# Optimization experiments

Hardware: AMD Instinct MI355X
Metric: run time of the kernel (lower is better)

## Reference

```python
import jax, jax.numpy as jnp
import numpy as np
import math

B, L, D, H = 2, 2048, 1024, 16
HD = D // H

def setup_inputs() -> dict:
    key = jax.random.key(0)
    ks = jax.random.split(key, 8)
    s = 1.0 / math.sqrt(D)
    # causal additive mask: 0 on/below diagonal, -inf above
    causal = jnp.where(jnp.tril(jnp.ones((L, L), dtype=bool)), 0.0, -jnp.inf)
    causal = causal[None, None].astype(jnp.float32)  # [1,1,L,L]
    return {
        "Q": jax.random.normal(ks[0], (B, L, D), jnp.float32),
        "K": jax.random.normal(ks[1], (B, L, D), jnp.float32),
        "V": jax.random.normal(ks[2], (B, L, D), jnp.float32),
        "attn_mask": causal,
        "padding_mask": jnp.zeros((B, L), dtype=bool),
        "wq": jax.random.normal(ks[3], (D, D), jnp.float32) * s,
        "wk": jax.random.normal(ks[4], (D, D), jnp.float32) * s,
        "wv": jax.random.normal(ks[5], (D, D), jnp.float32) * s,
        "wout": jax.random.normal(ks[6], (D, D), jnp.float32) * s,
    }

def reference(Q, K, V, attn_mask, padding_mask, wq, wk, wv, wout):
    b, l, _ = Q.shape
    # projections (torch Linear: x @ W.T); weights sampled as [out,in]-like square
    def proj(x, w):
        return (x @ w.T).reshape(b, l, H, HD).transpose(0, 2, 1, 3)  # [B,H,L,hd]
    q = proj(Q, wq)
    k = proj(K, wk)
    v = proj(V, wv)
    scores = jnp.einsum("bhqd,bhkd->bhqk", q, k) / math.sqrt(HD)
    scores = scores + attn_mask
    scores = jnp.where(padding_mask[:, None, None, :], -jnp.inf, scores)
    weights = jax.nn.softmax(scores, axis=-1)
    ctx = jnp.einsum("bhqk,bhkd->bhqd", weights, v)
    ctx = ctx.transpose(0, 2, 1, 3).reshape(b, l, D)
    return ctx @ wout.T
```

## Files before the change

kernel.cpp:

```cpp
#include <hip/hip_runtime.h>
#include <stdint.h>
#include <stddef.h>

typedef __bf16 bf16_t;
typedef bf16_t bf16x4 __attribute__((ext_vector_type(4)));
typedef bf16_t bf16x8 __attribute__((ext_vector_type(8)));
typedef float f32x4 __attribute__((ext_vector_type(4)));
typedef uint32_t u32x2 __attribute__((ext_vector_type(2)));
typedef uint32_t u32x4 __attribute__((ext_vector_type(4)));

#define MFMA_BF16(A_, B_, C_) __builtin_amdgcn_mfma_f32_16x16x32_bf16(A_, B_, C_, 0, 0, 0)

static constexpr int Lseq = 2048;
static constexpr int Dmod = 1024;
static constexpr int Hn   = 16;
static constexpr int HDim = 64;
static constexpr size_t M1 = 1u << 20;

__device__ __forceinline__ int swz(int row, int chunk) {
  return row * 64 + ((chunk ^ (row & 7)) << 3);
}

__device__ __forceinline__ void async_ld16(const bf16_t* g, bf16_t* l) {
  __builtin_amdgcn_global_load_lds(
      (const __attribute__((address_space(1))) void*)g,
      (__attribute__((address_space(3))) void*)l, 16, 0, 0);
}

__device__ __forceinline__ bf16x8 xpose(uint32_t a0, uint32_t a1,
                                        uint32_t b0, uint32_t b1,
                                        int s0, int s1, bool lo) {
  uint32_t ua0 = (uint32_t)__shfl((int)a0, s0, 64);
  uint32_t ub0 = (uint32_t)__shfl((int)b0, s0, 64);
  uint32_t ua1 = (uint32_t)__shfl((int)a1, s0, 64);
  uint32_t ub1 = (uint32_t)__shfl((int)b1, s0, 64);
  uint32_t va0 = (uint32_t)__shfl((int)a0, s1, 64);
  uint32_t vb0 = (uint32_t)__shfl((int)b0, s1, 64);
  uint32_t va1 = (uint32_t)__shfl((int)a1, s1, 64);
  uint32_t vb1 = (uint32_t)__shfl((int)b1, s1, 64);
  u32x4 t;
  t[0] = lo ? ua0 : ub0;
  t[1] = lo ? ua1 : ub1;
  t[2] = lo ? va0 : vb0;
  t[3] = lo ? va1 : vb1;
  return __builtin_bit_cast(bf16x8, t);
}

__device__ __forceinline__ u32x2 pack4(float e0, float e1, float e2, float e3) {
  bf16x4 p;
  p[0] = (bf16_t)e0; p[1] = (bf16_t)e1; p[2] = (bf16_t)e2; p[3] = (bf16_t)e3;
  return __builtin_bit_cast(u32x2, p);
}

__global__ __launch_bounds__(256) void cvt_kernel(
    const float* __restrict__ Q, const float* __restrict__ K,
    const float* __restrict__ V, const float* __restrict__ wq,
    const float* __restrict__ wk, const float* __restrict__ wv,
    const float* __restrict__ wout, bf16_t* __restrict__ wsb)
{
  const int s = blockIdx.z;
  const float* __restrict__ src;
  if      (s < 4)   src = Q    + (size_t)s * M1;
  else if (s < 8)   src = K    + (size_t)(s - 4) * M1;
  else if (s < 12)  src = V    + (size_t)(s - 8) * M1;
  else if (s == 12) src = wq;
  else if (s == 13) src = wk;
  else if (s == 14) src = wv;
  else              src = wout;
  bf16_t* __restrict__ dst = wsb + (size_t)s * M1;
  const float scale = (s == 12) ? 0.18033688f : 1.0f;

  const int idx = blockIdx.x * 256 + threadIdx.x;
  float4 a = ((const float4*)src)[idx * 2];
  float4 b = ((const float4*)src)[idx * 2 + 1];
  bf16x8 o;
  o[0] = (bf16_t)(a.x * scale); o[1] = (bf16_t)(a.y * scale);
  o[2] = (bf16_t)(a.z * scale); o[3] = (bf16_t)(a.w * scale);
  o[4] = (bf16_t)(b.x * scale); o[5] = (bf16_t)(b.y * scale);
  o[6] = (bf16_t)(b.z * scale); o[7] = (bf16_t)(b.w * scale);
  ((bf16x8*)dst)[idx] = o;
}

__global__ __launch_bounds__(256) void proj_kernel(
    const bf16_t* __restrict__ Qbf, const bf16_t* __restrict__ Kbf,
    const bf16_t* __restrict__ Vbf, const bf16_t* __restrict__ wqb,
    const bf16_t* __restrict__ wkb, const bf16_t* __restrict__ wvb,
    bf16_t* __restrict__ qo, bf16_t* __restrict__ ko, bf16_t* __restrict__ vo)
{
  const int z = blockIdx.z;
  const bf16_t* __restrict__ A  = (z == 0) ? Qbf : (z == 1) ? Kbf : Vbf;
  const bf16_t* __restrict__ Bw = (z == 0) ? wqb : (z == 1) ? wkb : wvb;
  bf16_t* __restrict__ dst      = (z == 0) ? qo  : (z == 1) ? ko  : vo;

  __shared__ __align__(16) bf16_t As[128 * 64];
  __shared__ __align__(16) bf16_t Bs[128 * 64];

  const int tid  = threadIdx.x;
  const int wave = tid >> 6;
  const int lane = tid & 63;
  const int quad = lane >> 4;
  const int l16  = lane & 15;
  const int wm   = (wave & 1) * 64;
  const int wn   = (wave >> 1) * 64;
  const int m0   = blockIdx.x * 128;
  const int n0   = blockIdx.y * 128;

  const int srow8  = lane >> 3;
  const int schunk = (lane & 7) ^ srow8;

  f32x4 acc[4][4];
#pragma unroll
  for (int i = 0; i < 4; ++i)
#pragma unroll
    for (int j = 0; j < 4; ++j)
#pragma unroll
      for (int e = 0; e < 4; ++e) acc[i][j][e] = 0.0f;

  for (int kt = 0; kt < 16; ++kt) {
    const int k0 = kt * 64;
    __syncthreads();
#pragma unroll
    for (int i = 0; i < 4; ++i) {
      const int rb = wave * 32 + i * 8;
      async_ld16(&A[(size_t)(m0 + rb + srow8) * Dmod + k0 + schunk * 8], &As[rb * 64]);
      async_ld16(&Bw[(size_t)(n0 + rb + srow8) * Dmod + k0 + schunk * 8], &Bs[rb * 64]);
    }
    __syncthreads();

    bf16x8 af[4][2], bfr[4][2];
#pragma unroll
    for (int mt = 0; mt < 4; ++mt) {
      const int row = wm + mt * 16 + l16;
      af[mt][0] = *(const bf16x8*)&As[swz(row, quad)];
      af[mt][1] = *(const bf16x8*)&As[swz(row, quad + 4)];
    }
#pragma unroll
    for (int nt = 0; nt < 4; ++nt) {
      const int row = wn + nt * 16 + l16;
      bfr[nt][0] = *(const bf16x8*)&Bs[swz(row, quad)];
      bfr[nt][1] = *(const bf16x8*)&Bs[swz(row, quad + 4)];
    }
#pragma unroll
    for (int mt = 0; mt < 4; ++mt)
#pragma unroll
      for (int nt = 0; nt < 4; ++nt) {
        acc[mt][nt] = MFMA_BF16(af[mt][0], bfr[nt][0], acc[mt][nt]);
        acc[mt][nt] = MFMA_BF16(af[mt][1], bfr[nt][1], acc[mt][nt]);
      }
  }

#pragma unroll
  for (int mt = 0; mt < 4; ++mt) {
    const int grb = m0 + wm + mt * 16 + quad * 4;
    const int bb  = grb >> 11;
    const int lb  = grb & 2047;
#pragma unroll
    for (int nt = 0; nt < 4; ++nt) {
      const int gc = n0 + wn + nt * 16 + l16;
      const int h  = gc >> 6;
      const int hd = gc & 63;
      if (z == 2) {
        bf16x4 pk;
#pragma unroll
        for (int r = 0; r < 4; ++r) pk[r] = (bf16_t)acc[mt][nt][r];
        *(bf16x4*)&dst[(((size_t)(bb * Hn + h) * HDim + hd) << 11) + lb] = pk;
      } else {
#pragma unroll
        for (int r = 0; r < 4; ++r)
          dst[(((size_t)(bb * Hn + h) * Lseq + lb + r) << 6) + hd] = (bf16_t)acc[mt][nt][r];
      }
    }
  }
}

__global__ __launch_bounds__(256, 4) void attn_kernel(
    const bf16_t* __restrict__ q, const bf16_t* __restrict__ k,
    const bf16_t* __restrict__ v, bf16_t* __restrict__ Op,
    float* __restrict__ Lp)
{
  const int id   = blockIdx.x;
  const int bh   = id & 31;
  const int sub  = id >> 5;
  const int qt   = 15 - (sub >> 1);
  const int half = sub & 1;
  const int q0   = qt * 128;
  const int jt0  = half * (qt + 1);
  const int jt1  = jt0 + qt;

  const int tid  = threadIdx.x;
  const int wave = tid >> 6;
  const int lane = tid & 63;
  const int quad = lane >> 4;
  const int l16  = lane & 15;

  __shared__ __align__(16) bf16_t Ks[2][64 * 64];
  __shared__ __align__(16) bf16_t Vs[2][64 * 64];

  const bf16_t* __restrict__ qb = q + (size_t)bh * (Lseq * HDim);
  const bf16_t* __restrict__ kb = k + (size_t)bh * (Lseq * HDim);
  const bf16_t* __restrict__ vb = v + (size_t)bh * (HDim * Lseq);

  const int srow8  = lane >> 3;
  const int schunk = (lane & 7) ^ srow8;

  bf16x8 ones;
#pragma unroll
  for (int i = 0; i < 8; ++i) ones[i] = (bf16_t)1.0f;

  const int qlo = q0 + wave * 32;
  const int qhi = qlo + 31;

  const int qrow0 = qlo + l16;
  bf16x8 qf00 = *(const bf16x8*)&qb[(size_t)qrow0 * HDim + quad * 8];
  bf16x8 qf01 = *(const bf16x8*)&qb[(size_t)qrow0 * HDim + 32 + quad * 8];
  bf16x8 qf10 = *(const bf16x8*)&qb[(size_t)(qrow0 + 16) * HDim + quad * 8];
  bf16x8 qf11 = *(const bf16x8*)&qb[(size_t)(qrow0 + 16) * HDim + 32 + quad * 8];

  const bf16_t* ks0 = kb + (size_t)(jt0 * 64 + wave * 16 + srow8) * HDim + schunk * 8;
  const bf16_t* ks1 = ks0 + (size_t)8 * HDim;
  const bf16_t* vs0 = vb + (size_t)(wave * 16 + srow8) * Lseq + jt0 * 64 + schunk * 8;
  const bf16_t* vs1 = vs0 + (size_t)8 * Lseq;
  const int ldo0 = (wave * 16) * 64;
  const int ldo1 = (wave * 16 + 8) * 64;

  int ro0[4], ro1[4];
#pragma unroll
  for (int nt = 0; nt < 4; ++nt) {
    const int row = nt * 16 + l16;
    ro0[nt] = swz(row, quad);
    ro1[nt] = swz(row, quad + 4);
  }

  const int ts0 = l16 + ((quad & 1) << 5);
  const int ts1 = ts0 + 16;
  const bool tlo = (quad < 2);

  f32x4 o0[4], o1[4];
  f32x4 lacc0, lacc1;
#pragma unroll
  for (int e = 0; e < 4; ++e) { lacc0[e] = 0.0f; lacc1[e] = 0.0f; }
#pragma unroll
  for (int nt = 0; nt < 4; ++nt)
#pragma unroll
    for (int e = 0; e < 4; ++e) { o0[nt][e] = 0.0f; o1[nt][e] = 0.0f; }

  async_ld16(ks0, &Ks[0][ldo0]);
  async_ld16(ks1, &Ks[0][ldo1]);
  async_ld16(vs0, &Vs[0][ldo0]);
  async_ld16(vs1, &Vs[0][ldo1]);
  ks0 += (size_t)64 * HDim; ks1 += (size_t)64 * HDim;
  vs0 += 64;                vs1 += 64;

  for (int jt = jt0; jt <= jt1; ++jt) {
    const int cur = (jt - jt0) & 1;
    __syncthreads();

    if (jt < jt1) {
      async_ld16(ks0, &Ks[cur ^ 1][ldo0]);
      async_ld16(ks1, &Ks[cur ^ 1][ldo1]);
      async_ld16(vs0, &Vs[cur ^ 1][ldo0]);
      async_ld16(vs1, &Vs[cur ^ 1][ldo1]);
      ks0 += (size_t)64 * HDim; ks1 += (size_t)64 * HDim;
      vs0 += 64;                vs1 += 64;
    }

    if (jt * 64 <= qhi) {
      const bool diag = (jt * 64 + 63 > qlo);

      uint32_t w0[4][2], w1[4][2];
      const int db0 = qlo + l16 - jt * 64;
      const int db1 = db0 + 16;

      if (diag) {
#pragma unroll
        for (int nt = 0; nt < 4; ++nt) {
          bf16x8 kf0 = *(const bf16x8*)&Ks[cur][ro0[nt]];
          bf16x8 kf1 = *(const bf16x8*)&Ks[cur][ro1[nt]];
          f32x4 s0, s1;
#pragma unroll
          for (int e = 0; e < 4; ++e) { s0[e] = 0.0f; s1[e] = 0.0f; }
          s0 = MFMA_BF16(kf0, qf00, s0);
          s0 = MFMA_BF16(kf1, qf01, s0);
          s1 = MFMA_BF16(kf0, qf10, s1);
          s1 = MFMA_BF16(kf1, qf11, s1);
          float e0[4], e1[4];
#pragma unroll
          for (int r = 0; r < 4; ++r) {
            const int kl = nt * 16 + quad * 4 + r;
            e0[r] = __builtin_amdgcn_exp2f((kl > db0) ? -1e30f : s0[r]);
            e1[r] = __builtin_amdgcn_exp2f((kl > db1) ? -1e30f : s1[r]);
          }
          u32x2 pa = pack4(e0[0], e0[1], e0[2], e0[3]);
          u32x2 pb = pack4(e1[0], e1[1], e1[2], e1[3]);
          w0[nt][0] = pa[0]; w0[nt][1] = pa[1];
          w1[nt][0] = pb[0]; w1[nt][1] = pb[1];
        }
      } else {
#pragma unroll
        for (int nt = 0; nt < 4; ++nt) {
          bf16x8 kf0 = *(const bf16x8*)&Ks[cur][ro0[nt]];
          bf16x8 kf1 = *(const bf16x8*)&Ks[cur][ro1[nt]];
          f32x4 s0, s1;
#pragma unroll
          for (int e = 0; e < 4; ++e) { s0[e] = 0.0f; s1[e] = 0.0f; }
          s0 = MFMA_BF16(kf0, qf00, s0);
          s0 = MFMA_BF16(kf1, qf01, s0);
          s1 = MFMA_BF16(kf0, qf10, s1);
          s1 = MFMA_BF16(kf1, qf11, s1);
          float e0[4], e1[4];
#pragma unroll
          for (int r = 0; r < 4; ++r) {
            e0[r] = __builtin_amdgcn_exp2f(s0[r]);
            e1[r] = __builtin_amdgcn_exp2f(s1[r]);
          }
          u32x2 pa = pack4(e0[0], e0[1], e0[2], e0[3]);
          u32x2 pb = pack4(e1[0], e1[1], e1[2], e1[3]);
          w0[nt][0] = pa[0]; w0[nt][1] = pa[1];
          w1[nt][0] = pb[0]; w1[nt][1] = pb[1];
        }
      }

      bf16x8 pf00 = xpose(w0[0][0], w0[0][1], w0[1][0], w0[1][1], ts0, ts1, tlo);
      bf16x8 pf01 = xpose(w0[2][0], w0[2][1], w0[3][0], w0[3][1], ts0, ts1, tlo);
      bf16x8 pf10 = xpose(w1[0][0], w1[0][1], w1[1][0], w1[1][1], ts0, ts1, tlo);
      bf16x8 pf11 = xpose(w1[2][0], w1[2][1], w1[3][0], w1[3][1], ts0, ts1, tlo);

      lacc0 = MFMA_BF16(pf00, ones, lacc0);
      lacc0 = MFMA_BF16(pf01, ones, lacc0);
      lacc1 = MFMA_BF16(pf10, ones, lacc1);
      lacc1 = MFMA_BF16(pf11, ones, lacc1);

#pragma unroll
      for (int nt = 0; nt < 4; ++nt) {
        bf16x8 vf0 = *(const bf16x8*)&Vs[cur][ro0[nt]];
        bf16x8 vf1 = *(const bf16x8*)&Vs[cur][ro1[nt]];
        o0[nt] = MFMA_BF16(pf00, vf0, o0[nt]);
        o0[nt] = MFMA_BF16(pf01, vf1, o0[nt]);
        o1[nt] = MFMA_BF16(pf10, vf0, o1[nt]);
        o1[nt] = MFMA_BF16(pf11, vf1, o1[nt]);
      }
    }
  }

  bf16_t* __restrict__ op = Op + ((size_t)half * 32 + bh) * Lseq * 64;
  float*  __restrict__ lp = Lp + ((size_t)half * 32 + bh) * Lseq;
#pragma unroll
  for (int nt = 0; nt < 4; ++nt)
#pragma unroll
    for (int r = 0; r < 4; ++r) {
      const int gq0 = q0 + wave * 32 + quad * 4 + r;
      const int gq1 = gq0 + 16;
      op[(size_t)gq0 * 64 + nt * 16 + l16] = (bf16_t)o0[nt][r];
      op[(size_t)gq1 * 64 + nt * 16 + l16] = (bf16_t)o1[nt][r];
    }
  if (l16 == 0) {
#pragma unroll
    for (int r = 0; r < 4; ++r) {
      const int gq0 = q0 + wave * 32 + quad * 4 + r;
      lp[gq0]      = lacc0[r];
      lp[gq0 + 16] = lacc1[r];
    }
  }
}

__global__ __launch_bounds__(256) void combine_kernel(
    const bf16_t* __restrict__ Op, const float* __restrict__ Lp,
    bf16_t* __restrict__ ctx)
{
  const int t   = blockIdx.x * 256 + threadIdx.x;
  const int d4  = t & 15;
  const int row = (t >> 4) & 2047;
  const int bh  = t >> 15;
  const size_t o_off = ((size_t)bh * Lseq + row) * 64 + d4 * 4;
  const bf16x4 a = *(const bf16x4*)&Op[o_off];
  const bf16x4 b = *(const bf16x4*)&Op[(size_t)32 * Lseq * 64 + o_off];
  const float  l = Lp[bh * Lseq + row] + Lp[32 * Lseq + bh * Lseq + row];
  const float inv = 1.0f / l;
  const int bb = bh >> 4, h = bh & 15;
  bf16x4 o4;
  o4[0] = (bf16_t)(((float)a[0] + (float)b[0]) * inv);
  o4[1] = (bf16_t)(((float)a[1] + (float)b[1]) * inv);
  o4[2] = (bf16_t)(((float)a[2] + (float)b[2]) * inv);
  o4[3] = (bf16_t)(((float)a[3] + (float)b[3]) * inv);
  *(bf16x4*)&ctx[(size_t)(bb * Lseq + row) * Dmod + h * HDim + d4 * 4] = o4;
}

__global__ __launch_bounds__(256) void out_kernel(
    const bf16_t* __restrict__ Actx, const bf16_t* __restrict__ Bwout,
    float* __restrict__ out)
{
  __shared__ __align__(16) bf16_t As[128 * 64];
  __shared__ __align__(16) bf16_t Bs[128 * 64];

  const int tid  = threadIdx.x;
  const int wave = tid >> 6;
  const int lane = tid & 63;
  const int quad = lane >> 4;
  const int l16  = lane & 15;
  const int wm   = (wave & 1) * 64;
  const int wn   = (wave >> 1) * 64;
  const int m0   = blockIdx.x * 128;
  const int n0   = blockIdx.y * 128;

  const int srow8  = lane >> 3;
  const int schunk = (lane & 7) ^ srow8;

  f32x4 acc[4][4];
#pragma unroll
  for (int i = 0; i < 4; ++i)
#pragma unroll
    for (int j = 0; j < 4; ++j)
#pragma unroll
      for (int e = 0; e < 4; ++e) acc[i][j][e] = 0.0f;

  for (int kt = 0; kt < 16; ++kt) {
    const int k0 = kt * 64;
    __syncthreads();
#pragma unroll
    for (int i = 0; i < 4; ++i) {
      const int rb = wave * 32 + i * 8;
      async_ld16(&Actx[(size_t)(m0 + rb + srow8) * Dmod + k0 + schunk * 8], &As[rb * 64]);
      async_ld16(&Bwout[(size_t)(n0 + rb + srow8) * Dmod + k0 + schunk * 8], &Bs[rb * 64]);
    }
    __syncthreads();

    bf16x8 af[4][2], bfr[4][2];
#pragma unroll
    for (int mt = 0; mt < 4; ++mt) {
      const int row = wm + mt * 16 + l16;
      af[mt][0] = *(const bf16x8*)&As[swz(row, quad)];
      af[mt][1] = *(const bf16x8*)&As[swz(row, quad + 4)];
    }
#pragma unroll
    for (int nt = 0; nt < 4; ++nt) {
      const int row = wn + nt * 16 + l16;
      bfr[nt][0] = *(const bf16x8*)&Bs[swz(row, quad)];
      bfr[nt][1] = *(const bf16x8*)&Bs[swz(row, quad + 4)];
    }
#pragma unroll
    for (int mt = 0; mt < 4; ++mt)
#pragma unroll
      for (int nt = 0; nt < 4; ++nt) {
        acc[mt][nt] = MFMA_BF16(af[mt][0], bfr[nt][0], acc[mt][nt]);
        acc[mt][nt] = MFMA_BF16(af[mt][1], bfr[nt][1], acc[mt][nt]);
      }
  }

#pragma unroll
  for (int mt = 0; mt < 4; ++mt) {
    const int grb = m0 + wm + mt * 16 + quad * 4;
#pragma unroll
    for (int nt = 0; nt < 4; ++nt) {
      const int gc = n0 + wn + nt * 16 + l16;
#pragma unroll
      for (int r = 0; r < 4; ++r)
        out[(size_t)(grb + r) * Dmod + gc] = acc[mt][nt][r];
    }
  }
}

extern "C" void kernel_launch(void* const* d_in, const int* in_sizes, int n_in,
                              void* d_out, int out_size, void* d_ws, size_t ws_size,
                              hipStream_t stream) {
  (void)in_sizes; (void)n_in; (void)out_size; (void)ws_size;
  const float* Q    = (const float*)d_in[0];
  const float* K    = (const float*)d_in[1];
  const float* V    = (const float*)d_in[2];
  const float* wq   = (const float*)d_in[5];
  const float* wk   = (const float*)d_in[6];
  const float* wv   = (const float*)d_in[7];
  const float* wout = (const float*)d_in[8];
  float* out = (float*)d_out;

  bf16_t* wsb = (bf16_t*)d_ws;
  bf16_t* Qbf   = wsb;
  bf16_t* Kbf   = wsb + 4 * M1;
  bf16_t* Vbf   = wsb + 8 * M1;
  bf16_t* wqb   = wsb + 12 * M1;
  bf16_t* wkb   = wsb + 13 * M1;
  bf16_t* wvb   = wsb + 14 * M1;
  bf16_t* woutb = wsb + 15 * M1;
  bf16_t* qp    = wsb + 16 * M1;
  bf16_t* kp    = wsb + 20 * M1;
  bf16_t* vp    = wsb + 24 * M1;
  bf16_t* Opart = wsb + 28 * M1;
  float*  Lpart = (float*)(wsb + 36 * M1);
  bf16_t* cws   = wsb;

  cvt_kernel<<<dim3(512, 1, 16), 256, 0, stream>>>(Q, K, V, wq, wk, wv, wout, wsb);
  proj_kernel<<<dim3(32, 8, 3), 256, 0, stream>>>(Qbf, Kbf, Vbf, wqb, wkb, wvb, qp, kp, vp);
  attn_kernel<<<dim3(1024), 256, 0, stream>>>(qp, kp, vp, Opart, Lpart);
  combine_kernel<<<dim3(4096), 256, 0, stream>>>(Opart, Lpart, cws);
  out_kernel<<<dim3(32, 8), 256, 0, stream>>>(cws, woutb, out);
}
```

Measured before the change: 223.1 us.

## Double-buffer GEMM tiles and drop split-KV attention with combine kernel

The projection and output GEMMs now use two LDS buffers, prefetching the next K-tile with async loads while the current one is computed, which removes one barrier per iteration. The attention kernel no longer splits each query tile's key range in half. Each block processes the full causal range, normalises by the row sum itself and writes ctx directly, so the separate combine kernel and the partial-output traffic are gone. In exchange attention launches half as many blocks with longer per-block work and worse load balance. The doubled shared memory in the GEMMs may also reduce occupancy.

```diff
diff --git a/kernel.cpp b/kernel.cpp
--- a/kernel.cpp
+++ b/kernel.cpp
@@ -92,8 +92,8 @@
   const bf16_t* __restrict__ Bw = (z == 0) ? wqb : (z == 1) ? wkb : wvb;
   bf16_t* __restrict__ dst      = (z == 0) ? qo  : (z == 1) ? ko  : vo;
 
-  __shared__ __align__(16) bf16_t As[128 * 64];
-  __shared__ __align__(16) bf16_t Bs[128 * 64];
+  __shared__ __align__(16) bf16_t As[2][128 * 64];
+  __shared__ __align__(16) bf16_t Bs[2][128 * 64];
 
   const int tid  = threadIdx.x;
   const int wave = tid >> 6;
@@ -116,29 +116,41 @@
 #pragma unroll
       for (int e = 0; e < 4; ++e) acc[i][j][e] = 0.0f;
 
+#pragma unroll
+  for (int i = 0; i < 4; ++i) {
+    const int rb = wave * 32 + i * 8;
+    async_ld16(&A[(size_t)(m0 + rb + srow8) * Dmod + schunk * 8], &As[0][rb * 64]);
+    async_ld16(&Bw[(size_t)(n0 + rb + srow8) * Dmod + schunk * 8], &Bs[0][rb * 64]);
+  }
+
   for (int kt = 0; kt < 16; ++kt) {
-    const int k0 = kt * 64;
+    const int cur = kt & 1;
     __syncthreads();
-#pragma unroll
-    for (int i = 0; i < 4; ++i) {
-      const int rb = wave * 32 + i * 8;
-      async_ld16(&A[(size_t)(m0 + rb + srow8) * Dmod + k0 + schunk * 8], &As[rb * 64]);
-      async_ld16(&Bw[(size_t)(n0 + rb + srow8) * Dmod + k0 + schunk * 8], &Bs[rb * 64]);
-    }
-    __syncthreads();
+
+    if (kt < 15) {
+      const int k0n = (kt + 1) * 64;
+#pragma unroll
+      for (int i = 0; i < 4; ++i) {
+        const int rb = wave * 32 + i * 8;
+        async_ld16(&A[(size_t)(m0 + rb + srow8) * Dmod + k0n + schunk * 8],
+                   &As[cur ^ 1][rb * 64]);
+        async_ld16(&Bw[(size_t)(n0 + rb + srow8) * Dmod + k0n + schunk * 8],
+                   &Bs[cur ^ 1][rb * 64]);
+      }
+    }
 
     bf16x8 af[4][2], bfr[4][2];
 #pragma unroll
     for (int mt = 0; mt < 4; ++mt) {
       const int row = wm + mt * 16 + l16;
-      af[mt][0] = *(const bf16x8*)&As[swz(row, quad)];
-      af[mt][1] = *(const bf16x8*)&As[swz(row, quad + 4)];
+      af[mt][0] = *(const bf16x8*)&As[cur][swz(row, quad)];
+      af[mt][1] = *(const bf16x8*)&As[cur][swz(row, quad + 4)];
     }
 #pragma unroll
     for (int nt = 0; nt < 4; ++nt) {
       const int row = wn + nt * 16 + l16;
-      bfr[nt][0] = *(const bf16x8*)&Bs[swz(row, quad)];
-      bfr[nt][1] = *(const bf16x8*)&Bs[swz(row, quad + 4)];
+      bfr[nt][0] = *(const bf16x8*)&Bs[cur][swz(row, quad)];
+      bfr[nt][1] = *(const bf16x8*)&Bs[cur][swz(row, quad + 4)];
     }
 #pragma unroll
     for (int mt = 0; mt < 4; ++mt)
@@ -175,17 +187,13 @@
 
 __global__ __launch_bounds__(256, 4) void attn_kernel(
     const bf16_t* __restrict__ q, const bf16_t* __restrict__ k,
-    const bf16_t* __restrict__ v, bf16_t* __restrict__ Op,
-    float* __restrict__ Lp)
+    const bf16_t* __restrict__ v, bf16_t* __restrict__ ctx)
 {
-  const int id   = blockIdx.x;
-  const int bh   = id & 31;
-  const int sub  = id >> 5;
-  const int qt   = 15 - (sub >> 1);
-  const int half = sub & 1;
-  const int q0   = qt * 128;
-  const int jt0  = half * (qt + 1);
-  const int jt1  = jt0 + qt;
+  const int bh = blockIdx.x;
+  const int qt = 15 - blockIdx.y;
+  const int bb = bh >> 4;
+  const int h  = bh & 15;
+  const int q0 = qt * 128;
 
   const int tid  = threadIdx.x;
   const int wave = tid >> 6;
@@ -216,9 +224,9 @@
   bf16x8 qf10 = *(const bf16x8*)&qb[(size_t)(qrow0 + 16) * HDim + quad * 8];
   bf16x8 qf11 = *(const bf16x8*)&qb[(size_t)(qrow0 + 16) * HDim + 32 + quad * 8];
 
-  const bf16_t* ks0 = kb + (size_t)(jt0 * 64 + wave * 16 + srow8) * HDim + schunk * 8;
+  const bf16_t* ks0 = kb + (size_t)(wave * 16 + srow8) * HDim + schunk * 8;
   const bf16_t* ks1 = ks0 + (size_t)8 * HDim;
-  const bf16_t* vs0 = vb + (size_t)(wave * 16 + srow8) * Lseq + jt0 * 64 + schunk * 8;
+  const bf16_t* vs0 = vb + (size_t)(wave * 16 + srow8) * Lseq + schunk * 8;
   const bf16_t* vs1 = vs0 + (size_t)8 * Lseq;
   const int ldo0 = (wave * 16) * 64;
   const int ldo1 = (wave * 16 + 8) * 64;
@@ -251,11 +259,12 @@
   ks0 += (size_t)64 * HDim; ks1 += (size_t)64 * HDim;
   vs0 += 64;                vs1 += 64;
 
-  for (int jt = jt0; jt <= jt1; ++jt) {
-    const int cur = (jt - jt0) & 1;
+  const int jtmax = 2 * qt + 1;
+  for (int jt = 0; jt <= jtmax; ++jt) {
+    const int cur = jt & 1;
     __syncthreads();
 
-    if (jt < jt1) {
+    if (jt < jtmax) {
       async_ld16(ks0, &Ks[cur ^ 1][ldo0]);
       async_ld16(ks1, &Ks[cur ^ 1][ldo1]);
       async_ld16(vs0, &Vs[cur ^ 1][ldo0]);
@@ -342,55 +351,31 @@
     }
   }
 
-  bf16_t* __restrict__ op = Op + ((size_t)half * 32 + bh) * Lseq * 64;
-  float*  __restrict__ lp = Lp + ((size_t)half * 32 + bh) * Lseq;
+  float inv0[4], inv1[4];
+#pragma unroll
+  for (int r = 0; r < 4; ++r) {
+    inv0[r] = 1.0f / lacc0[r];
+    inv1[r] = 1.0f / lacc1[r];
+  }
 #pragma unroll
   for (int nt = 0; nt < 4; ++nt)
 #pragma unroll
     for (int r = 0; r < 4; ++r) {
       const int gq0 = q0 + wave * 32 + quad * 4 + r;
       const int gq1 = gq0 + 16;
-      op[(size_t)gq0 * 64 + nt * 16 + l16] = (bf16_t)o0[nt][r];
-      op[(size_t)gq1 * 64 + nt * 16 + l16] = (bf16_t)o1[nt][r];
-    }
-  if (l16 == 0) {
-#pragma unroll
-    for (int r = 0; r < 4; ++r) {
-      const int gq0 = q0 + wave * 32 + quad * 4 + r;
-      lp[gq0]      = lacc0[r];
-      lp[gq0 + 16] = lacc1[r];
-    }
-  }
-}
-
-__global__ __launch_bounds__(256) void combine_kernel(
-    const bf16_t* __restrict__ Op, const float* __restrict__ Lp,
-    bf16_t* __restrict__ ctx)
-{
-  const int t   = blockIdx.x * 256 + threadIdx.x;
-  const int d4  = t & 15;
-  const int row = (t >> 4) & 2047;
-  const int bh  = t >> 15;
-  const size_t o_off = ((size_t)bh * Lseq + row) * 64 + d4 * 4;
-  const bf16x4 a = *(const bf16x4*)&Op[o_off];
-  const bf16x4 b = *(const bf16x4*)&Op[(size_t)32 * Lseq * 64 + o_off];
-  const float  l = Lp[bh * Lseq + row] + Lp[32 * Lseq + bh * Lseq + row];
-  const float inv = 1.0f / l;
-  const int bb = bh >> 4, h = bh & 15;
-  bf16x4 o4;
-  o4[0] = (bf16_t)(((float)a[0] + (float)b[0]) * inv);
-  o4[1] = (bf16_t)(((float)a[1] + (float)b[1]) * inv);
-  o4[2] = (bf16_t)(((float)a[2] + (float)b[2]) * inv);
-  o4[3] = (bf16_t)(((float)a[3] + (float)b[3]) * inv);
-  *(bf16x4*)&ctx[(size_t)(bb * Lseq + row) * Dmod + h * HDim + d4 * 4] = o4;
+      ctx[(size_t)(bb * Lseq + gq0) * Dmod + h * HDim + nt * 16 + l16] =
+          (bf16_t)(o0[nt][r] * inv0[r]);
+      ctx[(size_t)(bb * Lseq + gq1) * Dmod + h * HDim + nt * 16 + l16] =
+          (bf16_t)(o1[nt][r] * inv1[r]);
+    }
 }
 
 __global__ __launch_bounds__(256) void out_kernel(
     const bf16_t* __restrict__ Actx, const bf16_t* __restrict__ Bwout,
     float* __restrict__ out)
 {
-  __shared__ __align__(16) bf16_t As[128 * 64];
-  __shared__ __align__(16) bf16_t Bs[128 * 64];
+  __shared__ __align__(16) bf16_t As[2][128 * 64];
+  __shared__ __align__(16) bf16_t Bs[2][128 * 64];
 
   const int tid  = threadIdx.x;
   const int wave = tid >> 6;
@@ -413,29 +398,41 @@
 #pragma unroll
       for (int e = 0; e < 4; ++e) acc[i][j][e] = 0.0f;
 
+#pragma unroll
+  for (int i = 0; i < 4; ++i) {
+    const int rb = wave * 32 + i * 8;
+    async_ld16(&Actx[(size_t)(m0 + rb + srow8) * Dmod + schunk * 8], &As[0][rb * 64]);
+    async_ld16(&Bwout[(size_t)(n0 + rb + srow8) * Dmod + schunk * 8], &Bs[0][rb * 64]);
+  }
+
   for (int kt = 0; kt < 16; ++kt) {
-    const int k0 = kt * 64;
+    const int cur = kt & 1;
     __syncthreads();
-#pragma unroll
-    for (int i = 0; i < 4; ++i) {
-      const int rb = wave * 32 + i * 8;
-      async_ld16(&Actx[(size_t)(m0 + rb + srow8) * Dmod + k0 + schunk * 8], &As[rb * 64]);
-      async_ld16(&Bwout[(size_t)(n0 + rb + srow8) * Dmod + k0 + schunk * 8], &Bs[rb * 64]);
-    }
-    __syncthreads();
+
+    if (kt < 15) {
+      const int k0n = (kt + 1) * 64;
+#pragma unroll
+      for (int i = 0; i < 4; ++i) {
+        const int rb = wave * 32 + i * 8;
+        async_ld16(&Actx[(size_t)(m0 + rb + srow8) * Dmod + k0n + schunk * 8],
+                   &As[cur ^ 1][rb * 64]);
+        async_ld16(&Bwout[(size_t)(n0 + rb + srow8) * Dmod + k0n + schunk * 8],
+                   &Bs[cur ^ 1][rb * 64]);
+      }
+    }
 
     bf16x8 af[4][2], bfr[4][2];
 #pragma unroll
     for (int mt = 0; mt < 4; ++mt) {
       const int row = wm + mt * 16 + l16;
-      af[mt][0] = *(const bf16x8*)&As[swz(row, quad)];
-      af[mt][1] = *(const bf16x8*)&As[swz(row, quad + 4)];
+      af[mt][0] = *(const bf16x8*)&As[cur][swz(row, quad)];
+      af[mt][1] = *(const bf16x8*)&As[cur][swz(row, quad + 4)];
     }
 #pragma unroll
     for (int nt = 0; nt < 4; ++nt) {
       const int row = wn + nt * 16 + l16;
-      bfr[nt][0] = *(const bf16x8*)&Bs[swz(row, quad)];
-      bfr[nt][1] = *(const bf16x8*)&Bs[swz(row, quad + 4)];
+      bfr[nt][0] = *(const bf16x8*)&Bs[cur][swz(row, quad)];
+      bfr[nt][1] = *(const bf16x8*)&Bs[cur][swz(row, quad + 4)];
     }
 #pragma unroll
     for (int mt = 0; mt < 4; ++mt)
@@ -483,13 +480,10 @@
   bf16_t* qp    = wsb + 16 * M1;
   bf16_t* kp    = wsb + 20 * M1;
   bf16_t* vp    = wsb + 24 * M1;
-  bf16_t* Opart = wsb + 28 * M1;
-  float*  Lpart = (float*)(wsb + 36 * M1);
   bf16_t* cws   = wsb;
 
   cvt_kernel<<<dim3(512, 1, 16), 256, 0, stream>>>(Q, K, V, wq, wk, wv, wout, wsb);
   proj_kernel<<<dim3(32, 8, 3), 256, 0, stream>>>(Qbf, Kbf, Vbf, wqb, wkb, wvb, qp, kp, vp);
-  attn_kernel<<<dim3(1024), 256, 0, stream>>>(qp, kp, vp, Opart, Lpart);
-  combine_kernel<<<dim3(4096), 256, 0, stream>>>(Opart, Lpart, cws);
+  attn_kernel<<<dim3(32, 16), 256, 0, stream>>>(qp, kp, vp, cws);
   out_kernel<<<dim3(32, 8), 256, 0, stream>>>(cws, woutb, out);
 }
```

Result: slower. 232.5 us (+4.2%).
